# Optimization experiments

Hardware: AMD Instinct MI355X
Metric: run time of the kernel (lower is better)

## Reference

```python
import jax, jax.numpy as jnp
import numpy as np

GRID = 7          # grid_unit
NSAMPLE = 48      # sample_num
RADIUS = 0.3      # radiu_grid
FEAT = 128


def square_distance(src, dst):
    # src [B,N,C], dst [B,M,C] -> [B,N,M]
    d = -2.0 * jnp.einsum('bnc,bmc->bnm', src, dst)
    d = d + jnp.sum(src * src, -1)[:, :, None]
    d = d + jnp.sum(dst * dst, -1)[:, None, :]
    return d


def batch_norm(x):
    n = jnp.sqrt(jnp.sum(x * x, axis=2, keepdims=True) + 1e-8)
    return x / (n + 1e-10)


def query_ball_point(radius, nsample, xyz, new_xyz):
    B, N, _ = xyz.shape
    sqr = square_distance(new_xyz, xyz)                       # [B,S,N]
    gidx = jnp.where(sqr > radius ** 2, N, jnp.arange(N)[None, None, :])
    gidx = jnp.sort(gidx, axis=-1)[:, :, :nsample]            # [B,S,ns]
    first = gidx[:, :, :1]
    return jnp.where(gidx == N, first, gidx)


def index_points(points, idx):
    # points [B,N,C], idx [B,S,K] -> [B,S,K,C]
    return jax.vmap(lambda p, i: p[i])(points, idx)


def _forward(xyz, pts_feat, W0, b0, W1, b1, W_unet, index):
    B = xyz.shape[0]
    pts = jnp.transpose(xyz[:, 0:3, :], (0, 2, 1))            # [B,N,3]
    N = pts.shape[1]
    g = GRID

    # mlp0 / mlp1 (Conv1d(128,3,1)) + batch_norm
    oris = batch_norm(pts_feat @ W0.T + b0)                   # [B,N,3]
    nors = batch_norm(pts_feat @ W1.T + b1)                   # [B,N,3]

    # ---- rot_pts_3D ----
    gidx = query_ball_point(RADIUS, NSAMPLE, pts, pts)        # [B,N,48]
    group_pts = index_points(pts, gidx)                       # [B,N,48,3]
    group_feat = index_points(pts_feat, gidx).reshape(-1, NSAMPLE, FEAT)  # [BN,48,128]

    ori_rot90 = batch_norm(jnp.cross(oris, nors))
    ori_0 = batch_norm(jnp.cross(ori_rot90, nors))
    rot = jnp.concatenate([ori_0, ori_rot90, nors], axis=-1).reshape(-1, 3, 3)
    rot = jnp.transpose(rot, (0, 2, 1))                       # [BN,3,3]

    local = (group_pts - pts[:, :, None, :]).reshape(-1, NSAMPLE, 3)
    local_pts = jnp.einsum('bsc,bcd->bsd', local, rot)        # [BN,48,3]

    coords = jnp.round((local_pts + RADIUS) / (2 * RADIUS) * (g - 1)).astype(jnp.int32)
    coords = jnp.clip(coords, 0, g - 1)
    # faithful to the original flattening: x*g + y*g + z
    idx = coords[..., 0] * g + coords[..., 1] * g + coords[..., 2]  # [BN,48]

    BN = local_pts.shape[0]
    grid0 = jnp.zeros((BN, g * g * g, FEAT), dtype=pts_feat.dtype)
    feat3d = grid0.at[jnp.arange(BN)[:, None], idx].set(group_feat)  # [BN,343,128]

    # ---- UNet3D stand-in: [BN,128,7,7,7] -> [BN,3,7,7] via (channel,depth) projection
    feat5d = feat3d.reshape(BN, g, g, g, FEAT)
    feat_off = jnp.einsum('bijkc,ckd->bijd', feat5d, W_unet).reshape(BN, g * g, 3)

    # ---- rot_offset ----
    vals = jnp.array([[i * 0.01, j * 0.01, 0.0]
                      for i in range(-30, 36, 10)
                      for j in range(-30, 36, 10)], dtype=pts.dtype)   # [49,3]
    up = vals[None] + feat_off                                # [BN,49,3]
    pts_repeat = pts.reshape(-1, 1, 3)                        # [BN,1,3]
    pts_up = jnp.einsum('bsc,bdc->bsd', up, rot) + pts_repeat  # v @ rot^T

    pts_offset = pts_up[:, 24, :].reshape(B, -1, 3)           # [B,N,3]
    pts_ups = pts_up[:, index, :].reshape(B, -1, 3)           # [B,16N,3]
    return (oris, nors, pts_ups, pts_offset, pts_up)


def setup_inputs() -> dict:
    key = jax.random.key(0)
    ks = jax.random.split(key, 6)
    B, N, C = 2, 1024, 128
    xyz = jax.random.normal(ks[0], (B, 3, N), dtype=jnp.float32)
    pts_feat = jax.random.normal(ks[1], (B, N, C), dtype=jnp.float32)
    W0 = jax.random.normal(ks[2], (3, C), dtype=jnp.float32) * 0.05
    b0 = jnp.zeros((3,), dtype=jnp.float32)
    W1 = jax.random.normal(ks[3], (3, C), dtype=jnp.float32) * 0.05
    b1 = jnp.zeros((3,), dtype=jnp.float32)
    W_unet = jax.random.normal(ks[4], (C, GRID, 3), dtype=jnp.float32) * 0.02
    index = jax.random.randint(ks[5], (16,), 0, GRID * GRID)
    return {"xyz": xyz, "pts_feat": pts_feat, "W0": W0, "b0": b0,
            "W1": W1, "b1": b1, "W_unet": W_unet, "index": index}


def reference(xyz, pts_feat, W0, b0, W1, b1, W_unet, index):
    return _forward(xyz, pts_feat, W0, b0, W1, b1, W_unet, index)
```

## Files before the change

kernel.cpp:

```cpp
#include <hip/hip_runtime.h>

#define NB 2
#define NP 1024
#define NC 128
#define NG 7
#define NSM 48
#define BN (NB*NP)

#define OFF_ORIS 0
#define OFF_NORS (BN*3)
#define OFF_PUPS (2*BN*3)
#define OFF_POFF (OFF_PUPS + BN*16*3)
#define OFF_PU   (OFF_POFF + BN*3)

__device__ __forceinline__ void bnorm3(float v[3]) {
    float ss = __fadd_rn(__fadd_rn(__fmul_rn(v[0],v[0]), __fmul_rn(v[1],v[1])), __fmul_rn(v[2],v[2]));
    float nr = sqrtf(__fadd_rn(ss, 1e-8f));
    float dn = __fadd_rn(nr, 1e-10f);
    v[0] = __fdiv_rn(v[0], dn);
    v[1] = __fdiv_rn(v[1], dn);
    v[2] = __fdiv_rn(v[2], dn);
}

__global__ __launch_bounds__(256) void kfused(const float* __restrict__ xyz,
                                              const float* __restrict__ feat,
                                              const float* __restrict__ W0, const float* __restrict__ b0,
                                              const float* __restrict__ W1, const float* __restrict__ b1,
                                              const float* __restrict__ W_unet,
                                              const int* __restrict__ index,
                                              float* __restrict__ out) {
    __shared__ float spts[NP*3];
    __shared__ float snrm[NP];
    __shared__ float srot[9];
    __shared__ unsigned long long smask[16];
    __shared__ int   sgidx[NSM];
    __shared__ int   sidx[NSM];
    __shared__ int   swin[NSM];
    __shared__ int   scnt;
    __shared__ float sfo[NG*NG*3];
    __shared__ float spu[NG*NG*3];

    int p = blockIdx.x;
    int b = p >> 10, n = p & (NP - 1);
    int tid = threadIdx.x;
    int w = tid >> 6, l = tid & 63;

    if (tid < NG*NG*3) sfo[tid] = 0.0f;

    if (w == 0) {
        float f0 = feat[p*NC + l];
        float f1 = feat[p*NC + 64 + l];
        float s0 = f0*W0[l]     + f1*W0[64+l];
        float s1 = f0*W0[128+l] + f1*W0[192+l];
        float s2 = f0*W0[256+l] + f1*W0[320+l];
        float s3 = f0*W1[l]     + f1*W1[64+l];
        float s4 = f0*W1[128+l] + f1*W1[192+l];
        float s5 = f0*W1[256+l] + f1*W1[320+l];
        for (int off = 32; off; off >>= 1) {
            s0 += __shfl_xor(s0, off);
            s1 += __shfl_xor(s1, off);
            s2 += __shfl_xor(s2, off);
            s3 += __shfl_xor(s3, off);
            s4 += __shfl_xor(s4, off);
            s5 += __shfl_xor(s5, off);
        }
        if (l == 0) {
            float o[3]  = { s0 + b0[0], s1 + b0[1], s2 + b0[2] };
            float nn[3] = { s3 + b1[0], s4 + b1[1], s5 + b1[2] };
            bnorm3(o);
            bnorm3(nn);
            float r90[3];
            r90[0] = __fsub_rn(__fmul_rn(o[1], nn[2]), __fmul_rn(o[2], nn[1]));
            r90[1] = __fsub_rn(__fmul_rn(o[2], nn[0]), __fmul_rn(o[0], nn[2]));
            r90[2] = __fsub_rn(__fmul_rn(o[0], nn[1]), __fmul_rn(o[1], nn[0]));
            bnorm3(r90);
            float o0[3];
            o0[0] = __fsub_rn(__fmul_rn(r90[1], nn[2]), __fmul_rn(r90[2], nn[1]));
            o0[1] = __fsub_rn(__fmul_rn(r90[2], nn[0]), __fmul_rn(r90[0], nn[2]));
            o0[2] = __fsub_rn(__fmul_rn(r90[0], nn[1]), __fmul_rn(r90[1], nn[0]));
            bnorm3(o0);

            out[OFF_ORIS + p*3+0] = o[0];  out[OFF_ORIS + p*3+1] = o[1];  out[OFF_ORIS + p*3+2] = o[2];
            out[OFF_NORS + p*3+0] = nn[0]; out[OFF_NORS + p*3+1] = nn[1]; out[OFF_NORS + p*3+2] = nn[2];

            srot[0] = o0[0];  srot[1] = o0[1];  srot[2] = o0[2];
            srot[3] = r90[0]; srot[4] = r90[1]; srot[5] = r90[2];
            srot[6] = nn[0];  srot[7] = nn[1];  srot[8] = nn[2];
        }
    } else {
        const float* xb = xyz + (size_t)b*3*NP;
        for (int j = tid - 64; j < NP; j += 192) {
            float px = xb[j];
            float py = xb[NP + j];
            float pz = xb[2*NP + j];
            spts[j*3+0] = px; spts[j*3+1] = py; spts[j*3+2] = pz;
            snrm[j] = __fadd_rn(__fadd_rn(__fmul_rn(px,px), __fmul_rn(py,py)), __fmul_rn(pz,pz));
        }
    }
    __syncthreads();

    {
        float cx = spts[n*3+0], cy = spts[n*3+1], cz = spts[n*3+2];
        float cn = snrm[n];
        #pragma unroll
        for (int k = 0; k < 4; ++k) {
            int m = ((w<<2) + k)*64 + l;
            float dot = __fadd_rn(__fadd_rn(__fmul_rn(cx, spts[m*3+0]),
                                            __fmul_rn(cy, spts[m*3+1])),
                                  __fmul_rn(cz, spts[m*3+2]));
            float d = __fadd_rn(__fadd_rn(__fmul_rn(-2.0f, dot), cn), snrm[m]);
            bool sel = !(d > 0.09f);
            unsigned long long mk = __ballot(sel);
            if (l == 0) smask[(w<<2) + k] = mk;
        }
    }
    __syncthreads();

    if (tid < 16) {
        unsigned long long wv = smask[tid];
        int prefix = 0, total = 0;
        #pragma unroll
        for (int j = 0; j < 16; ++j) {
            int pc = __popcll(smask[j]);
            if (j < tid) prefix += pc;
            total += pc;
        }
        if (tid == 0) scnt = total;
        int pos = prefix;
        while (wv && pos < NSM) {
            int bpos = __ffsll(wv) - 1;
            sgidx[pos++] = (tid << 6) + bpos;
            wv &= wv - 1;
        }
    }
    __syncthreads();

    {
        int total = scnt;
        if (tid < NSM && tid >= total) sgidx[tid] = sgidx[0];
    }
    __syncthreads();

    if (tid < NSM) {
        int m = sgidx[tid];
        float lx = spts[m*3+0] - spts[n*3+0];
        float ly = spts[m*3+1] - spts[n*3+1];
        float lz = spts[m*3+2] - spts[n*3+2];
        int c[3];
        #pragma unroll
        for (int dd = 0; dd < 3; ++dd) {
            float lp = __fadd_rn(__fadd_rn(__fmul_rn(lx, srot[dd*3+0]),
                                           __fmul_rn(ly, srot[dd*3+1])),
                                 __fmul_rn(lz, srot[dd*3+2]));
            float t = rintf(__fmul_rn(__fdiv_rn(__fadd_rn(lp, 0.3f), 0.6f), 6.0f));
            int ci = (int)t;
            ci = ci < 0 ? 0 : (ci > 6 ? 6 : ci);
            c[dd] = ci;
        }
        sidx[tid] = c[0]*NG + c[1]*NG + c[2];
    }
    __syncthreads();

    if (tid < NSM) {
        int win = 1, my = sidx[tid];
        for (int s2 = tid + 1; s2 < NSM; ++s2)
            if (sidx[s2] == my) { win = 0; break; }
        swin[tid] = win;
    }
    __syncthreads();

    {
        int sl = tid & 15;
        int sg = tid >> 4;
        #pragma unroll
        for (int r = 0; r < 3; ++r) {
            int s = r*16 + sg;
            int act = swin[s];
            int q = 0, k = 0;
            float p0 = 0.f, p1 = 0.f, p2 = 0.f;
            if (act) {
                int cell = sidx[s];
                k = cell % NG;
                q = cell / NG;
                const float* fr = feat + (size_t)(b*NP + sgidx[s]) * NC;
                #pragma unroll
                for (int c8 = 0; c8 < 8; ++c8) {
                    int cc = sl + c8*16;
                    float f = fr[cc];
                    const float* wp = W_unet + cc*(NG*3) + k*3;
                    p0 += f * wp[0];
                    p1 += f * wp[1];
                    p2 += f * wp[2];
                }
            }
            #pragma unroll
            for (int off = 8; off; off >>= 1) {
                p0 += __shfl_xor(p0, off);
                p1 += __shfl_xor(p1, off);
                p2 += __shfl_xor(p2, off);
            }
            if (act && sl == 0) {
                atomicAdd(&sfo[q*3+0], p0);
                atomicAdd(&sfo[q*3+1], p1);
                atomicAdd(&sfo[q*3+2], p2);
            }
        }
    }
    __syncthreads();

    if (tid < NG*NG*3) {
        int q = tid / 3, d = tid % 3;
        int qi = q / NG, qj = q % NG;
        float v0 = (float)((-30 + 10*qi) * 0.01);
        float v1 = (float)((-30 + 10*qj) * 0.01);
        float u0 = __fadd_rn(v0, sfo[q*3+0]);
        float u1 = __fadd_rn(v1, sfo[q*3+1]);
        float u2 = sfo[q*3+2];
        float r = __fadd_rn(
                    __fadd_rn(
                      __fadd_rn(__fmul_rn(u0, srot[0*3+d]), __fmul_rn(u1, srot[1*3+d])),
                      __fmul_rn(u2, srot[2*3+d])),
                    spts[n*3+d]);
        spu[tid] = r;
        out[OFF_PU + p*(NG*NG*3) + tid] = r;
        if (q == 24) out[OFF_POFF + p*3 + d] = r;
    }
    __syncthreads();

    if (tid < 16*3) {
        int t = tid / 3, d = tid % 3;
        int q = index[t];
        out[OFF_PUPS + (p*16 + t)*3 + d] = spu[q*3 + d];
    }
}

extern "C" void kernel_launch(void* const* d_in, const int* in_sizes, int n_in,
                              void* d_out, int out_size, void* d_ws, size_t ws_size,
                              hipStream_t stream) {
    const float* xyz    = (const float*)d_in[0];
    const float* feat   = (const float*)d_in[1];
    const float* W0     = (const float*)d_in[2];
    const float* b0     = (const float*)d_in[3];
    const float* W1     = (const float*)d_in[4];
    const float* b1     = (const float*)d_in[5];
    const float* W_unet = (const float*)d_in[6];
    const int*   index  = (const int*)d_in[7];
    float* out = (float*)d_out;

    hipLaunchKernelGGL(kfused, dim3(BN), dim3(256), 0, stream,
                       xyz, feat, W0, b0, W1, b1, W_unet, index, out);
}
```

Baseline: 78.80 us.

## Drop shared point staging; compute ball-query distances directly from global xyz

Removes the per-block copy of all 1024 points and their norms into shared memory. Each wave now reads xyz straight from global (L2-resident) memory and computes distances in place, with wave 0 handling chunk 0 after the MLP step. The per-sample winner detection moves from an O(48^2) duplicate scan to an atomicMax into a per-cell table, and the first-index fill merges into the compaction step, which removes two block barriers. Shared-memory use drops sharply, which may allow more blocks per CU, at the cost of uncoalesced-stride global reads per block.

```diff
diff --git a/kernel.cpp b/kernel.cpp
--- a/kernel.cpp
+++ b/kernel.cpp
@@ -29,14 +29,11 @@
                                               const float* __restrict__ W_unet,
                                               const int* __restrict__ index,
                                               float* __restrict__ out) {
-    __shared__ float spts[NP*3];
-    __shared__ float snrm[NP];
     __shared__ float srot[9];
     __shared__ unsigned long long smask[16];
     __shared__ int   sgidx[NSM];
     __shared__ int   sidx[NSM];
-    __shared__ int   swin[NSM];
-    __shared__ int   scnt;
+    __shared__ int   scell[91];
     __shared__ float sfo[NG*NG*3];
     __shared__ float spu[NG*NG*3];
 
@@ -44,8 +41,13 @@
     int b = p >> 10, n = p & (NP - 1);
     int tid = threadIdx.x;
     int w = tid >> 6, l = tid & 63;
+    const float* xb = xyz + (size_t)b*3*NP;
 
     if (tid < NG*NG*3) sfo[tid] = 0.0f;
+    if (tid < 91)      scell[tid] = -1;
+
+    float cx = xb[n], cy = xb[NP + n], cz = xb[2*NP + n];
+    float cn = __fadd_rn(__fadd_rn(__fmul_rn(cx,cx), __fmul_rn(cy,cy)), __fmul_rn(cz,cz));
 
     if (w == 0) {
         float f0 = feat[p*NC + l];
@@ -87,65 +89,60 @@
             srot[3] = r90[0]; srot[4] = r90[1]; srot[5] = r90[2];
             srot[6] = nn[0];  srot[7] = nn[1];  srot[8] = nn[2];
         }
+        {
+            int m = l;
+            float mx = xb[m], my = xb[NP + m], mz = xb[2*NP + m];
+            float mn = __fadd_rn(__fadd_rn(__fmul_rn(mx,mx), __fmul_rn(my,my)), __fmul_rn(mz,mz));
+            float dot = __fadd_rn(__fadd_rn(__fmul_rn(cx,mx), __fmul_rn(cy,my)), __fmul_rn(cz,mz));
+            float d = __fadd_rn(__fadd_rn(__fmul_rn(-2.0f, dot), cn), mn);
+            unsigned long long mk = __ballot(!(d > 0.09f));
+            if (l == 0) smask[0] = mk;
+        }
     } else {
-        const float* xb = xyz + (size_t)b*3*NP;
-        for (int j = tid - 64; j < NP; j += 192) {
-            float px = xb[j];
-            float py = xb[NP + j];
-            float pz = xb[2*NP + j];
-            spts[j*3+0] = px; spts[j*3+1] = py; spts[j*3+2] = pz;
-            snrm[j] = __fadd_rn(__fadd_rn(__fmul_rn(px,px), __fmul_rn(py,py)), __fmul_rn(pz,pz));
-        }
-    }
-    __syncthreads();
-
-    {
-        float cx = spts[n*3+0], cy = spts[n*3+1], cz = spts[n*3+2];
-        float cn = snrm[n];
-        #pragma unroll
-        for (int k = 0; k < 4; ++k) {
-            int m = ((w<<2) + k)*64 + l;
-            float dot = __fadd_rn(__fadd_rn(__fmul_rn(cx, spts[m*3+0]),
-                                            __fmul_rn(cy, spts[m*3+1])),
-                                  __fmul_rn(cz, spts[m*3+2]));
-            float d = __fadd_rn(__fadd_rn(__fmul_rn(-2.0f, dot), cn), snrm[m]);
-            bool sel = !(d > 0.09f);
-            unsigned long long mk = __ballot(sel);
-            if (l == 0) smask[(w<<2) + k] = mk;
+        int ch0 = (w - 1) * 5 + 1;
+        #pragma unroll
+        for (int k = 0; k < 5; ++k) {
+            int ch = ch0 + k;
+            int m = (ch << 6) + l;
+            float mx = xb[m], my = xb[NP + m], mz = xb[2*NP + m];
+            float mn = __fadd_rn(__fadd_rn(__fmul_rn(mx,mx), __fmul_rn(my,my)), __fmul_rn(mz,mz));
+            float dot = __fadd_rn(__fadd_rn(__fmul_rn(cx,mx), __fmul_rn(cy,my)), __fmul_rn(cz,mz));
+            float d = __fadd_rn(__fadd_rn(__fmul_rn(-2.0f, dot), cn), mn);
+            unsigned long long mk = __ballot(!(d > 0.09f));
+            if (l == 0) smask[ch] = mk;
         }
     }
     __syncthreads();
 
     if (tid < 16) {
         unsigned long long wv = smask[tid];
-        int prefix = 0, total = 0;
+        int prefix = 0, total = 0, firstj = 0;
+        bool seen = false;
         #pragma unroll
         for (int j = 0; j < 16; ++j) {
             int pc = __popcll(smask[j]);
             if (j < tid) prefix += pc;
+            if (!seen && pc) { firstj = j; seen = true; }
             total += pc;
         }
-        if (tid == 0) scnt = total;
         int pos = prefix;
         while (wv && pos < NSM) {
             int bpos = __ffsll(wv) - 1;
             sgidx[pos++] = (tid << 6) + bpos;
             wv &= wv - 1;
         }
-    }
-    __syncthreads();
-
-    {
-        int total = scnt;
-        if (tid < NSM && tid >= total) sgidx[tid] = sgidx[0];
+        if (total < NSM) {
+            int first = (firstj << 6) + (__ffsll(smask[firstj]) - 1);
+            for (int q2 = total + tid; q2 < NSM; q2 += 16) sgidx[q2] = first;
+        }
     }
     __syncthreads();
 
     if (tid < NSM) {
         int m = sgidx[tid];
-        float lx = spts[m*3+0] - spts[n*3+0];
-        float ly = spts[m*3+1] - spts[n*3+1];
-        float lz = spts[m*3+2] - spts[n*3+2];
+        float lx = __fsub_rn(xb[m],        cx);
+        float ly = __fsub_rn(xb[NP + m],   cy);
+        float lz = __fsub_rn(xb[2*NP + m], cz);
         int c[3];
         #pragma unroll
         for (int dd = 0; dd < 3; ++dd) {
@@ -157,15 +154,9 @@
             ci = ci < 0 ? 0 : (ci > 6 ? 6 : ci);
             c[dd] = ci;
         }
-        sidx[tid] = c[0]*NG + c[1]*NG + c[2];
-    }
-    __syncthreads();
-
-    if (tid < NSM) {
-        int win = 1, my = sidx[tid];
-        for (int s2 = tid + 1; s2 < NSM; ++s2)
-            if (sidx[s2] == my) { win = 0; break; }
-        swin[tid] = win;
+        int cell = c[0]*NG + c[1]*NG + c[2];
+        sidx[tid] = cell;
+        atomicMax(&scell[cell], tid);
     }
     __syncthreads();
 
@@ -175,14 +166,12 @@
         #pragma unroll
         for (int r = 0; r < 3; ++r) {
             int s = r*16 + sg;
-            int act = swin[s];
-            int q = 0, k = 0;
-            float p0 = 0.f, p1 = 0.f, p2 = 0.f;
-            if (act) {
-                int cell = sidx[s];
-                k = cell % NG;
-                q = cell / NG;
+            int cell = sidx[s];
+            if (scell[cell] == s) {
+                int k = cell % NG;
+                int q = cell / NG;
                 const float* fr = feat + (size_t)(b*NP + sgidx[s]) * NC;
+                float p0 = 0.f, p1 = 0.f, p2 = 0.f;
                 #pragma unroll
                 for (int c8 = 0; c8 < 8; ++c8) {
                     int cc = sl + c8*16;
@@ -192,17 +181,17 @@
                     p1 += f * wp[1];
                     p2 += f * wp[2];
                 }
-            }
-            #pragma unroll
-            for (int off = 8; off; off >>= 1) {
-                p0 += __shfl_xor(p0, off);
-                p1 += __shfl_xor(p1, off);
-                p2 += __shfl_xor(p2, off);
-            }
-            if (act && sl == 0) {
-                atomicAdd(&sfo[q*3+0], p0);
-                atomicAdd(&sfo[q*3+1], p1);
-                atomicAdd(&sfo[q*3+2], p2);
+                #pragma unroll
+                for (int off = 8; off; off >>= 1) {
+                    p0 += __shfl_xor(p0, off);
+                    p1 += __shfl_xor(p1, off);
+                    p2 += __shfl_xor(p2, off);
+                }
+                if (sl == 0) {
+                    atomicAdd(&sfo[q*3+0], p0);
+                    atomicAdd(&sfo[q*3+1], p1);
+                    atomicAdd(&sfo[q*3+2], p2);
+                }
             }
         }
     }
@@ -216,11 +205,12 @@
         float u0 = __fadd_rn(v0, sfo[q*3+0]);
         float u1 = __fadd_rn(v1, sfo[q*3+1]);
         float u2 = sfo[q*3+2];
+        float ctr = (d == 0) ? cx : (d == 1) ? cy : cz;
         float r = __fadd_rn(
                     __fadd_rn(
                       __fadd_rn(__fmul_rn(u0, srot[0*3+d]), __fmul_rn(u1, srot[1*3+d])),
                       __fmul_rn(u2, srot[2*3+d])),
-                    spts[n*3+d]);
+                    ctr);
         spu[tid] = r;
         out[OFF_PU + p*(NG*NG*3) + tid] = r;
         if (q == 24) out[OFF_POFF + p*3 + d] = r;
```

After: 78.70 us, median of 2. About the same (-0.1%).
